# Kernel optimization log

Measured on AMD Instinct MI355X. Metric: run time of the kernel, lower is better.

## Reference

```python
import jax, jax.numpy as jnp
import numpy as np

B, T = 64, 4096
K = 67            # 25 body + 21 + 21 hand keypoints
D = 256           # first_layer_size
C = 7             # num_classes
THR = 0.1         # confidence_threshold
EPS = 1e-5        # BatchNorm eps


def setup_inputs() -> dict:
    key = jax.random.key(0)
    ks = jax.random.split(key, 8)
    body = jax.random.normal(ks[0], (B, T, 75), dtype=jnp.float32)
    hand_right = jax.random.normal(ks[1], (B, T, 63), dtype=jnp.float32)
    hand_left = jax.random.normal(ks[2], (B, T, 63), dtype=jnp.float32)
    length = jax.random.randint(ks[3], (B,), 1, T + 1, dtype=jnp.int64)
    W1 = jax.random.normal(ks[4], (2 * K, D), dtype=jnp.float32) * 0.05
    b1 = jnp.zeros((D,), dtype=jnp.float32)
    gamma = jnp.ones((D,), dtype=jnp.float32)
    beta = jnp.zeros((D,), dtype=jnp.float32)
    Wc = jax.random.normal(ks[5], (D, C), dtype=jnp.float32) * 0.05
    bc = jnp.zeros((C,), dtype=jnp.float32)
    return {"body": body, "hand_right": hand_right, "hand_left": hand_left,
            "length": length, "W1": W1, "b1": b1, "gamma": gamma,
            "beta": beta, "Wc": Wc, "bc": bc}


def reference(body, hand_right, hand_left, length, W1, b1, gamma, beta, Wc, bc):
    # concat keypoint streams -> [B, T, 3K] -> [B, T, K, 3]
    feats = jnp.concatenate([body, hand_right, hand_left], axis=2)
    feats = feats.reshape(feats.shape[0], feats.shape[1], -1, 3)
    x, y, conf = feats[..., 0], feats[..., 1], feats[..., 2]
    conf = (conf > THR).astype(feats.dtype)
    # gate coords by confidence, flatten to [B, T, 2K]
    pos = jnp.stack([x * conf, y * conf], axis=3)
    pos = pos.reshape(pos.shape[0], pos.shape[1], -1)
    # static MLP: Linear + ReLU -> [B, T, D]
    sf = jax.nn.relu(jnp.einsum("btf,fd->btd", pos, W1) + b1)
    # masked max pool over valid timesteps (vectorized segment-max)
    mask = jnp.arange(sf.shape[1])[None, :] < length[:, None]      # [B, T]
    pooled = jnp.max(jnp.where(mask[:, :, None], sf, -jnp.inf), axis=1)  # [B, D]
    # BatchNorm1d (training mode: batch statistics)
    mean = pooled.mean(axis=0)
    var = pooled.var(axis=0)
    bn = (pooled - mean) / jnp.sqrt(var + EPS) * gamma + beta
    # classifier
    return bn @ Wc + bc
```

## Files before the change

kernel.cpp:

```cpp
#include <hip/hip_runtime.h>
#include <hip/hip_bf16.h>

#define B_   64
#define T_   4096
#define K_   67
#define F_   134
#define FP_  160
#define D_   256
#define C_   7
#define THR_ 0.1f
#define EPS_ 1e-5f

typedef __bf16 bf16x8 __attribute__((ext_vector_type(8)));
typedef float  f32x4  __attribute__((ext_vector_type(4)));

typedef __attribute__((address_space(1))) const unsigned int guint;
typedef __attribute__((address_space(3))) unsigned int luint;


__device__ __forceinline__ int get_len(const int* L, int b) {
    return (L[1] == 0) ? L[2 * b] : L[b];
}

__global__ void convert_w1(const float* __restrict__ W1, __bf16* __restrict__ W1bf) {
    __shared__ float tile[32][33];
    const int d0 = blockIdx.x * 32, f0 = blockIdx.y * 32;
    const int tx = threadIdx.x & 31, ty = threadIdx.x >> 5;
#pragma unroll
    for (int r = 0; r < 32; r += 8) {
        int f = f0 + ty + r;
        tile[ty + r][tx] = (f < F_) ? W1[f * D_ + d0 + tx] : 0.f;
    }
    __syncthreads();
#pragma unroll
    for (int r = 0; r < 32; r += 8) {
        int d = d0 + ty + r;
        W1bf[d * FP_ + f0 + tx] = (__bf16)tile[tx][ty + r];
    }
}

__global__ __launch_bounds__(256, 3)
void fused_mlp_pool(const float* __restrict__ body,
                    const float* __restrict__ hr,
                    const float* __restrict__ hl,
                    const int*   __restrict__ length,
                    const float* __restrict__ b1,
                    const __bf16* __restrict__ W1bf,
                    float* __restrict__ pooled)
{
    const int b = blockIdx.y;
    const int len = get_len(length, b);
    const int t0 = blockIdx.x * 32;
    if (t0 >= len) return;

    __shared__ __align__(16) float  raw[6432];
    __shared__ __align__(16) __bf16 As[10 * 512];

    const int tid  = threadIdx.x;
    const int wave = tid >> 6;
    const int lane = tid & 63;
    const int quad = lane >> 4;
    const int l16  = lane & 15;
    const int dbase = wave * 64;

    const long rowb = (long)b * T_;
    const float* bodyt = body + (rowb + t0) * 75;
    const float* hrt   = hr   + (rowb + t0) * 63;
    const float* hlt   = hl   + (rowb + t0) * 63;

    for (int i = wave; i < 9; i += 4)
        __builtin_amdgcn_global_load_lds(
            (guint*)(bodyt + i * 256 + lane * 4),
            (luint*)((char*)raw + i * 1024 + lane * 16), 16, 0, 0);
    for (int i = wave; i < 7; i += 4)
        __builtin_amdgcn_global_load_lds(
            (guint*)(hrt + i * 256 + lane * 4),
            (luint*)((char*)raw + 9600 + i * 1024 + lane * 16), 16, 0, 0);
    for (int i = wave; i < 7; i += 4)
        __builtin_amdgcn_global_load_lds(
            (guint*)(hlt + i * 256 + lane * 4),
            (luint*)((char*)raw + 17664 + i * 1024 + lane * 16), 16, 0, 0);

    if (tid < 136) {
        const float* g; int loff;
        if (tid < 24)      { g = bodyt + 2304 + tid * 4;        loff = 2304 + tid * 4; }
        else if (tid < 80) { g = hrt + 1792 + (tid - 24) * 4;   loff = 4192 + (tid - 24) * 4; }
        else               { g = hlt + 1792 + (tid - 80) * 4;   loff = 6208 + (tid - 80) * 4; }
        *(float4*)(raw + loff) = *(const float4*)g;
    }

    bf16x8 bfrag[4][5];
    float  b1v[4];
#pragma unroll
    for (int n = 0; n < 4; n++) {
        int d = dbase + n * 16 + l16;
        const __bf16* p = W1bf + d * FP_ + quad * 8;
#pragma unroll
        for (int kt = 0; kt < 5; kt++)
            bfrag[n][kt] = *(const bf16x8*)(p + kt * 32);
        b1v[n] = b1[d];
    }

    for (int i = tid; i < 416; i += 256) {
        int t = i & 31, kp = 67 + (i >> 5);
        int w = ((t >> 4) * 5 + (kp >> 4)) * 256 + (((kp >> 2) & 3) * 16 + (t & 15)) * 4 + (kp & 3);
        ((unsigned int*)As)[w] = 0u;
    }
    __syncthreads();

#pragma unroll
    for (int it = 0; it < 8; it++) {
        int idx = it * 256 + tid;
        int t = (((idx >> 5) & 3) << 3) | ((idx >> 2) & 7);
        int k = (((idx >> 7) & 15) << 2) | (idx & 3);
        int roff;
        if (k < 25)      roff = t * 75 + 3 * k;
        else if (k < 46) roff = 2400 + t * 63 + 3 * (k - 25);
        else             roff = 4416 + t * 63 + 3 * (k - 46);
        float x = raw[roff], y = raw[roff + 1], cf = raw[roff + 2];
        if (!(cf > THR_)) { x = 0.f; y = 0.f; }
        unsigned short ux = __builtin_bit_cast(unsigned short, (__bf16)x);
        unsigned short uy = __builtin_bit_cast(unsigned short, (__bf16)y);
        int w = ((t >> 4) * 5 + (k >> 4)) * 256 + (((k >> 2) & 3) * 16 + (t & 15)) * 4 + (k & 3);
        ((unsigned int*)As)[w] = (unsigned int)ux | ((unsigned int)uy << 16);
    }
    if (tid < 96) {
        int t = tid & 31, k = 64 + (tid >> 5);
        int roff = 4416 + t * 63 + 3 * (k - 46);
        float x = raw[roff], y = raw[roff + 1], cf = raw[roff + 2];
        if (!(cf > THR_)) { x = 0.f; y = 0.f; }
        unsigned short ux = __builtin_bit_cast(unsigned short, (__bf16)x);
        unsigned short uy = __builtin_bit_cast(unsigned short, (__bf16)y);
        int w = ((t >> 4) * 5 + (k >> 4)) * 256 + (((k >> 2) & 3) * 16 + (t & 15)) * 4 + (k & 3);
        ((unsigned int*)As)[w] = (unsigned int)ux | ((unsigned int)uy << 16);
    }
    __syncthreads();

    f32x4 acc[2][4];
#pragma unroll
    for (int m = 0; m < 2; m++)
#pragma unroll
        for (int n = 0; n < 4; n++)
            acc[m][n] = (f32x4){0.f, 0.f, 0.f, 0.f};

#pragma unroll
    for (int kt = 0; kt < 5; kt++) {
#pragma unroll
        for (int m = 0; m < 2; m++) {
            bf16x8 a = *(const bf16x8*)(As + (m * 5 + kt) * 512 + lane * 8);
#pragma unroll
            for (int n = 0; n < 4; n++)
                acc[m][n] = __builtin_amdgcn_mfma_f32_16x16x32_bf16(a, bfrag[n][kt], acc[m][n], 0, 0, 0);
        }
    }

    float runmax[4] = {0.f, 0.f, 0.f, 0.f};
#pragma unroll
    for (int m = 0; m < 2; m++) {
        int trow0 = t0 + m * 16 + quad * 4;
#pragma unroll
        for (int r = 0; r < 4; r++) {
            bool valid = (trow0 + r) < len;
#pragma unroll
            for (int n = 0; n < 4; n++) {
                float v = acc[m][n][r] + b1v[n];
                v = (v > 0.f) ? v : 0.f;
                runmax[n] = (valid && v > runmax[n]) ? v : runmax[n];
            }
        }
    }
#pragma unroll
    for (int n = 0; n < 4; n++) {
        float r = runmax[n];
        r = fmaxf(r, __shfl_xor(r, 16, 64));
        r = fmaxf(r, __shfl_xor(r, 32, 64));
        if (quad == n) {
            atomicMax((unsigned int*)(pooled + b * D_ + dbase + n * 16 + l16),
                      __float_as_uint(r));
        }
    }
}

__global__ void bn_classifier(const float* __restrict__ pooled,
                              const float* __restrict__ gamma,
                              const float* __restrict__ beta,
                              const float* __restrict__ Wc,
                              const float* __restrict__ bc,
                              float* __restrict__ out)
{
    __shared__ float scale_s[D_], shift_s[D_];
    const int tid = threadIdx.x;
    float s = 0.f, ss = 0.f;
#pragma unroll 8
    for (int b = 0; b < B_; b++) {
        float v = pooled[b * D_ + tid];
        s += v; ss += v * v;
    }
    float mean = s * (1.f / B_);
    float var  = ss * (1.f / B_) - mean * mean;
    var = fmaxf(var, 0.f);
    float sc = gamma[tid] * rsqrtf(var + EPS_);
    scale_s[tid] = sc;
    shift_s[tid] = beta[tid] - mean * sc;

    const int wv = tid >> 6, ln = tid & 63;
    float wcr[4][C_];
#pragma unroll
    for (int j = 0; j < 4; j++)
#pragma unroll
        for (int c = 0; c < C_; c++)
            wcr[j][c] = Wc[(ln * 4 + j) * C_ + c];
    __syncthreads();

    for (int b = wv * 16; b < wv * 16 + 16; b++) {
        float4 v = *(const float4*)(pooled + b * D_ + ln * 4);
        float q[4];
        q[0] = v.x * scale_s[ln * 4 + 0] + shift_s[ln * 4 + 0];
        q[1] = v.y * scale_s[ln * 4 + 1] + shift_s[ln * 4 + 1];
        q[2] = v.z * scale_s[ln * 4 + 2] + shift_s[ln * 4 + 2];
        q[3] = v.w * scale_s[ln * 4 + 3] + shift_s[ln * 4 + 3];
        float p[C_];
#pragma unroll
        for (int c = 0; c < C_; c++) p[c] = 0.f;
#pragma unroll
        for (int j = 0; j < 4; j++)
#pragma unroll
            for (int c = 0; c < C_; c++)
                p[c] += q[j] * wcr[j][c];
#pragma unroll
        for (int c = 0; c < C_; c++) {
#pragma unroll
            for (int off = 1; off < 64; off <<= 1)
                p[c] += __shfl_xor(p[c], off, 64);
        }
        if (ln == 0) {
#pragma unroll
            for (int c = 0; c < C_; c++)
                out[b * C_ + c] = p[c] + bc[c];
        }
    }
}

extern "C" void kernel_launch(void* const* d_in, const int* in_sizes, int n_in,
                              void* d_out, int out_size, void* d_ws, size_t ws_size,
                              hipStream_t stream) {
    const float* body   = (const float*)d_in[0];
    const float* hr     = (const float*)d_in[1];
    const float* hl     = (const float*)d_in[2];
    const int*   length = (const int*)  d_in[3];
    const float* W1     = (const float*)d_in[4];
    const float* b1     = (const float*)d_in[5];
    const float* gamma  = (const float*)d_in[6];
    const float* beta   = (const float*)d_in[7];
    const float* Wc     = (const float*)d_in[8];
    const float* bc     = (const float*)d_in[9];
    float* out = (float*)d_out;

    float*  pooled = (float*)d_ws;
    __bf16* W1bf   = (__bf16*)((char*)d_ws + 65536);

    hipMemsetAsync(d_ws, 0, 65536, stream);
    convert_w1<<<dim3(8, 5), dim3(256), 0, stream>>>(W1, W1bf);
    fused_mlp_pool<<<dim3(128, B_), dim3(256), 0, stream>>>(body, hr, hl, length, b1, W1bf, pooled);
    bn_classifier<<<dim3(1), dim3(256), 0, stream>>>(pooled, gamma, beta, Wc, bc, out);
}
```

Measured before the change: 235.9 us.

## Use persistent grid over compacted valid tile list with amortized weight loads

Adds a small kernel that builds a compact list of valid (batch, time-tile) pairs from the lengths. The main kernel becomes a persistent grid of 1024 blocks that loops over this list. W1 fragments and bias are loaded once per block instead of once per tile, and blocks that would exit early are no longer launched. Occupancy hint raised to 4 blocks per CU. This adds an extra serial launch, and load/compute within a block are no longer overlapped across tiles.

Result: slower. 266.3 us (+12.9%).

```diff
diff --git a/kernel.cpp b/kernel.cpp
--- a/kernel.cpp
+++ b/kernel.cpp
@@ -10,6 +10,7 @@
 #define C_   7
 #define THR_ 0.1f
 #define EPS_ 1e-5f
+#define GRID_ 1024
 
 typedef __bf16 bf16x8 __attribute__((ext_vector_type(8)));
 typedef float  f32x4  __attribute__((ext_vector_type(4)));
@@ -39,22 +40,45 @@
     }
 }
 
-__global__ __launch_bounds__(256, 3)
+__global__ void build_tiles(const int* __restrict__ L,
+                            unsigned short* __restrict__ list,
+                            int* __restrict__ count) {
+    __shared__ int pref[65];
+    const int tid = threadIdx.x;
+    if (tid == 0) {
+        int acc = 0;
+        pref[0] = 0;
+        for (int b = 0; b < B_; b++) {
+            int len = (L[1] == 0) ? L[2 * b] : L[b];
+            acc += (len + 31) >> 5;
+            pref[b + 1] = acc;
+        }
+        *count = acc;
+    }
+    __syncthreads();
+    const int total = pref[64];
+    for (int i = tid; i < total; i += blockDim.x) {
+        int lo = 0, hi = 64;
+        while (hi - lo > 1) { int mid = (lo + hi) >> 1;
+                              if (pref[mid] <= i) lo = mid; else hi = mid; }
+        list[i] = (unsigned short)((lo << 7) | (i - pref[lo]));
+    }
+}
+
+__global__ __launch_bounds__(256, 4)
 void fused_mlp_pool(const float* __restrict__ body,
                     const float* __restrict__ hr,
                     const float* __restrict__ hl,
                     const int*   __restrict__ length,
                     const float* __restrict__ b1,
                     const __bf16* __restrict__ W1bf,
+                    const unsigned short* __restrict__ list,
+                    const int* __restrict__ count,
                     float* __restrict__ pooled)
 {
-    const int b = blockIdx.y;
-    const int len = get_len(length, b);
-    const int t0 = blockIdx.x * 32;
-    if (t0 >= len) return;
-
     __shared__ __align__(16) float  raw[6432];
     __shared__ __align__(16) __bf16 As[10 * 512];
+    __shared__ int len_s[B_];
 
     const int tid  = threadIdx.x;
     const int wave = tid >> 6;
@@ -63,31 +87,7 @@
     const int l16  = lane & 15;
     const int dbase = wave * 64;
 
-    const long rowb = (long)b * T_;
-    const float* bodyt = body + (rowb + t0) * 75;
-    const float* hrt   = hr   + (rowb + t0) * 63;
-    const float* hlt   = hl   + (rowb + t0) * 63;
-
-    for (int i = wave; i < 9; i += 4)
-        __builtin_amdgcn_global_load_lds(
-            (guint*)(bodyt + i * 256 + lane * 4),
-            (luint*)((char*)raw + i * 1024 + lane * 16), 16, 0, 0);
-    for (int i = wave; i < 7; i += 4)
-        __builtin_amdgcn_global_load_lds(
-            (guint*)(hrt + i * 256 + lane * 4),
-            (luint*)((char*)raw + 9600 + i * 1024 + lane * 16), 16, 0, 0);
-    for (int i = wave; i < 7; i += 4)
-        __builtin_amdgcn_global_load_lds(
-            (guint*)(hlt + i * 256 + lane * 4),
-            (luint*)((char*)raw + 17664 + i * 1024 + lane * 16), 16, 0, 0);
-
-    if (tid < 136) {
-        const float* g; int loff;
-        if (tid < 24)      { g = bodyt + 2304 + tid * 4;        loff = 2304 + tid * 4; }
-        else if (tid < 80) { g = hrt + 1792 + (tid - 24) * 4;   loff = 4192 + (tid - 24) * 4; }
-        else               { g = hlt + 1792 + (tid - 80) * 4;   loff = 6208 + (tid - 80) * 4; }
-        *(float4*)(raw + loff) = *(const float4*)g;
-    }
+    if (tid < B_) len_s[tid] = get_len(length, tid);
 
     bf16x8 bfrag[4][5];
     float  b1v[4];
@@ -106,77 +106,110 @@
         int w = ((t >> 4) * 5 + (kp >> 4)) * 256 + (((kp >> 2) & 3) * 16 + (t & 15)) * 4 + (kp & 3);
         ((unsigned int*)As)[w] = 0u;
     }
-    __syncthreads();
-
-#pragma unroll
-    for (int it = 0; it < 8; it++) {
-        int idx = it * 256 + tid;
-        int t = (((idx >> 5) & 3) << 3) | ((idx >> 2) & 7);
-        int k = (((idx >> 7) & 15) << 2) | (idx & 3);
-        int roff;
-        if (k < 25)      roff = t * 75 + 3 * k;
-        else if (k < 46) roff = 2400 + t * 63 + 3 * (k - 25);
-        else             roff = 4416 + t * 63 + 3 * (k - 46);
-        float x = raw[roff], y = raw[roff + 1], cf = raw[roff + 2];
-        if (!(cf > THR_)) { x = 0.f; y = 0.f; }
-        unsigned short ux = __builtin_bit_cast(unsigned short, (__bf16)x);
-        unsigned short uy = __builtin_bit_cast(unsigned short, (__bf16)y);
-        int w = ((t >> 4) * 5 + (k >> 4)) * 256 + (((k >> 2) & 3) * 16 + (t & 15)) * 4 + (k & 3);
-        ((unsigned int*)As)[w] = (unsigned int)ux | ((unsigned int)uy << 16);
-    }
-    if (tid < 96) {
-        int t = tid & 31, k = 64 + (tid >> 5);
-        int roff = 4416 + t * 63 + 3 * (k - 46);
-        float x = raw[roff], y = raw[roff + 1], cf = raw[roff + 2];
-        if (!(cf > THR_)) { x = 0.f; y = 0.f; }
-        unsigned short ux = __builtin_bit_cast(unsigned short, (__bf16)x);
-        unsigned short uy = __builtin_bit_cast(unsigned short, (__bf16)y);
-        int w = ((t >> 4) * 5 + (k >> 4)) * 256 + (((k >> 2) & 3) * 16 + (t & 15)) * 4 + (k & 3);
-        ((unsigned int*)As)[w] = (unsigned int)ux | ((unsigned int)uy << 16);
-    }
-    __syncthreads();
-
-    f32x4 acc[2][4];
-#pragma unroll
-    for (int m = 0; m < 2; m++)
-#pragma unroll
-        for (int n = 0; n < 4; n++)
-            acc[m][n] = (f32x4){0.f, 0.f, 0.f, 0.f};
-
-#pragma unroll
-    for (int kt = 0; kt < 5; kt++) {
+
+    const int total = *count;
+    for (int i = blockIdx.x; i < total; i += GRID_) {
+        const int e  = list[i];
+        const int b  = e >> 7;
+        const int t0 = (e & 127) << 5;
+        const long rowb = (long)b * T_;
+        const float* bodyt = body + (rowb + t0) * 75;
+        const float* hrt   = hr   + (rowb + t0) * 63;
+        const float* hlt   = hl   + (rowb + t0) * 63;
+
+        for (int k = wave; k < 9; k += 4)
+            __builtin_amdgcn_global_load_lds(
+                (guint*)(bodyt + k * 256 + lane * 4),
+                (luint*)((char*)raw + k * 1024 + lane * 16), 16, 0, 0);
+        for (int k = wave; k < 7; k += 4)
+            __builtin_amdgcn_global_load_lds(
+                (guint*)(hrt + k * 256 + lane * 4),
+                (luint*)((char*)raw + 9600 + k * 1024 + lane * 16), 16, 0, 0);
+        for (int k = wave; k < 7; k += 4)
+            __builtin_amdgcn_global_load_lds(
+                (guint*)(hlt + k * 256 + lane * 4),
+                (luint*)((char*)raw + 17664 + k * 1024 + lane * 16), 16, 0, 0);
+
+        if (tid < 136) {
+            const float* g; int loff;
+            if (tid < 24)      { g = bodyt + 2304 + tid * 4;        loff = 2304 + tid * 4; }
+            else if (tid < 80) { g = hrt + 1792 + (tid - 24) * 4;   loff = 4192 + (tid - 24) * 4; }
+            else               { g = hlt + 1792 + (tid - 80) * 4;   loff = 6208 + (tid - 80) * 4; }
+            *(float4*)(raw + loff) = *(const float4*)g;
+        }
+        __syncthreads();
+
+#pragma unroll
+        for (int it = 0; it < 8; it++) {
+            int idx = it * 256 + tid;
+            int t = (((idx >> 5) & 3) << 3) | ((idx >> 2) & 7);
+            int k = (((idx >> 7) & 15) << 2) | (idx & 3);
+            int roff;
+            if (k < 25)      roff = t * 75 + 3 * k;
+            else if (k < 46) roff = 2400 + t * 63 + 3 * (k - 25);
+            else             roff = 4416 + t * 63 + 3 * (k - 46);
+            float x = raw[roff], y = raw[roff + 1], cf = raw[roff + 2];
+            if (!(cf > THR_)) { x = 0.f; y = 0.f; }
+            unsigned short ux = __builtin_bit_cast(unsigned short, (__bf16)x);
+            unsigned short uy = __builtin_bit_cast(unsigned short, (__bf16)y);
+            int w = ((t >> 4) * 5 + (k >> 4)) * 256 + (((k >> 2) & 3) * 16 + (t & 15)) * 4 + (k & 3);
+            ((unsigned int*)As)[w] = (unsigned int)ux | ((unsigned int)uy << 16);
+        }
+        if (tid < 96) {
+            int t = tid & 31, k = 64 + (tid >> 5);
+            int roff = 4416 + t * 63 + 3 * (k - 46);
+            float x = raw[roff], y = raw[roff + 1], cf = raw[roff + 2];
+            if (!(cf > THR_)) { x = 0.f; y = 0.f; }
+            unsigned short ux = __builtin_bit_cast(unsigned short, (__bf16)x);
+            unsigned short uy = __builtin_bit_cast(unsigned short, (__bf16)y);
+            int w = ((t >> 4) * 5 + (k >> 4)) * 256 + (((k >> 2) & 3) * 16 + (t & 15)) * 4 + (k & 3);
+            ((unsigned int*)As)[w] = (unsigned int)ux | ((unsigned int)uy << 16);
+        }
+        __syncthreads();
+
+        f32x4 acc[2][4];
+#pragma unroll
+        for (int m = 0; m < 2; m++)
+#pragma unroll
+            for (int n = 0; n < 4; n++)
+                acc[m][n] = (f32x4){0.f, 0.f, 0.f, 0.f};
+
+#pragma unroll
+        for (int kt = 0; kt < 5; kt++) {
+#pragma unroll
+            for (int m = 0; m < 2; m++) {
+                bf16x8 a = *(const bf16x8*)(As + (m * 5 + kt) * 512 + lane * 8);
+#pragma unroll
+                for (int n = 0; n < 4; n++)
+                    acc[m][n] = __builtin_amdgcn_mfma_f32_16x16x32_bf16(a, bfrag[n][kt], acc[m][n], 0, 0, 0);
+            }
+        }
+
+        const int len = len_s[b];
+        float runmax[4] = {0.f, 0.f, 0.f, 0.f};
 #pragma unroll
         for (int m = 0; m < 2; m++) {
-            bf16x8 a = *(const bf16x8*)(As + (m * 5 + kt) * 512 + lane * 8);
-#pragma unroll
-            for (int n = 0; n < 4; n++)
-                acc[m][n] = __builtin_amdgcn_mfma_f32_16x16x32_bf16(a, bfrag[n][kt], acc[m][n], 0, 0, 0);
-        }
-    }
-
-    float runmax[4] = {0.f, 0.f, 0.f, 0.f};
-#pragma unroll
-    for (int m = 0; m < 2; m++) {
-        int trow0 = t0 + m * 16 + quad * 4;
-#pragma unroll
-        for (int r = 0; r < 4; r++) {
-            bool valid = (trow0 + r) < len;
-#pragma unroll
-            for (int n = 0; n < 4; n++) {
-                float v = acc[m][n][r] + b1v[n];
-                v = (v > 0.f) ? v : 0.f;
-                runmax[n] = (valid && v > runmax[n]) ? v : runmax[n];
+            int trow0 = t0 + m * 16 + quad * 4;
+#pragma unroll
+            for (int r = 0; r < 4; r++) {
+                bool valid = (trow0 + r) < len;
+#pragma unroll
+                for (int n = 0; n < 4; n++) {
+                    float v = acc[m][n][r] + b1v[n];
+                    v = (v > 0.f) ? v : 0.f;
+                    runmax[n] = (valid && v > runmax[n]) ? v : runmax[n];
+                }
             }
         }
-    }
-#pragma unroll
-    for (int n = 0; n < 4; n++) {
-        float r = runmax[n];
-        r = fmaxf(r, __shfl_xor(r, 16, 64));
-        r = fmaxf(r, __shfl_xor(r, 32, 64));
-        if (quad == n) {
-            atomicMax((unsigned int*)(pooled + b * D_ + dbase + n * 16 + l16),
-                      __float_as_uint(r));
+#pragma unroll
+        for (int n = 0; n < 4; n++) {
+            float r = runmax[n];
+            r = fmaxf(r, __shfl_xor(r, 16, 64));
+            r = fmaxf(r, __shfl_xor(r, 32, 64));
+            if (quad == n) {
+                atomicMax((unsigned int*)(pooled + b * D_ + dbase + n * 16 + l16),
+                          __float_as_uint(r));
+            }
         }
     }
 }
@@ -256,11 +289,15 @@
     const float* bc     = (const float*)d_in[9];
     float* out = (float*)d_out;
 
-    float*  pooled = (float*)d_ws;
-    __bf16* W1bf   = (__bf16*)((char*)d_ws + 65536);
+    float*          pooled = (float*)d_ws;
+    __bf16*         W1bf   = (__bf16*)((char*)d_ws + 65536);
+    unsigned short* list   = (unsigned short*)((char*)d_ws + 147456);
+    int*            count  = (int*)((char*)d_ws + 163840);
 
     hipMemsetAsync(d_ws, 0, 65536, stream);
     convert_w1<<<dim3(8, 5), dim3(256), 0, stream>>>(W1, W1bf);
-    fused_mlp_pool<<<dim3(128, B_), dim3(256), 0, stream>>>(body, hr, hl, length, b1, W1bf, pooled);
+    build_tiles<<<dim3(1), dim3(256), 0, stream>>>(length, list, count);
+    fused_mlp_pool<<<dim3(GRID_), dim3(256), 0, stream>>>(body, hr, hl, length, b1,
+                                                          W1bf, list, count, pooled);
     bn_classifier<<<dim3(1), dim3(256), 0, stream>>>(pooled, gamma, beta, Wc, bc, out);
 }
```

## Process four time tiles per block with double-buffered async LDS prefetch

Applied to the files above, without the earlier changes.

Each block now walks up to four 32-timestep chunks instead of one. While the current chunk is converted to bf16 and run through MFMA, the next chunk's keypoint data is prefetched into a second LDS buffer. This amortizes the W1 fragment loads, the bias loads and the per-block atomicMax over more work, and overlaps global loads with compute. In exchange LDS use doubles and occupancy is lowered to two blocks per CU. With four times fewer blocks there is also less parallelism and coarser load balance across batches of varying length.

Result: slower. 246.0 us (+4.2%).

```diff
diff --git a/kernel.cpp b/kernel.cpp
--- a/kernel.cpp
+++ b/kernel.cpp
@@ -10,6 +10,7 @@
 #define C_   7
 #define THR_ 0.1f
 #define EPS_ 1e-5f
+#define TPB_ 4
 
 typedef __bf16 bf16x8 __attribute__((ext_vector_type(8)));
 typedef float  f32x4  __attribute__((ext_vector_type(4)));
@@ -39,7 +40,7 @@
     }
 }
 
-__global__ __launch_bounds__(256, 3)
+__global__ __launch_bounds__(256, 2)
 void fused_mlp_pool(const float* __restrict__ body,
                     const float* __restrict__ hr,
                     const float* __restrict__ hl,
@@ -50,10 +51,11 @@
 {
     const int b = blockIdx.y;
     const int len = get_len(length, b);
-    const int t0 = blockIdx.x * 32;
-    if (t0 >= len) return;
-
-    __shared__ __align__(16) float  raw[6432];
+    const int cbase = blockIdx.x * (TPB_ * 32);
+    if (cbase >= len) return;
+    const int nt = min(TPB_, (len - cbase + 31) >> 5);
+
+    __shared__ __align__(16) float  raw[2][6432];
     __shared__ __align__(16) __bf16 As[10 * 512];
 
     const int tid  = threadIdx.x;
@@ -64,30 +66,34 @@
     const int dbase = wave * 64;
 
     const long rowb = (long)b * T_;
-    const float* bodyt = body + (rowb + t0) * 75;
-    const float* hrt   = hr   + (rowb + t0) * 63;
-    const float* hlt   = hl   + (rowb + t0) * 63;
-
-    for (int i = wave; i < 9; i += 4)
-        __builtin_amdgcn_global_load_lds(
-            (guint*)(bodyt + i * 256 + lane * 4),
-            (luint*)((char*)raw + i * 1024 + lane * 16), 16, 0, 0);
-    for (int i = wave; i < 7; i += 4)
-        __builtin_amdgcn_global_load_lds(
-            (guint*)(hrt + i * 256 + lane * 4),
-            (luint*)((char*)raw + 9600 + i * 1024 + lane * 16), 16, 0, 0);
-    for (int i = wave; i < 7; i += 4)
-        __builtin_amdgcn_global_load_lds(
-            (guint*)(hlt + i * 256 + lane * 4),
-            (luint*)((char*)raw + 17664 + i * 1024 + lane * 16), 16, 0, 0);
-
-    if (tid < 136) {
-        const float* g; int loff;
-        if (tid < 24)      { g = bodyt + 2304 + tid * 4;        loff = 2304 + tid * 4; }
-        else if (tid < 80) { g = hrt + 1792 + (tid - 24) * 4;   loff = 4192 + (tid - 24) * 4; }
-        else               { g = hlt + 1792 + (tid - 80) * 4;   loff = 6208 + (tid - 80) * 4; }
-        *(float4*)(raw + loff) = *(const float4*)g;
-    }
+
+    auto issue = [&](int tt, float* rbuf) {
+        const float* bt = body + (rowb + cbase + tt * 32) * 75;
+        const float* ht = hr   + (rowb + cbase + tt * 32) * 63;
+        const float* lt = hl   + (rowb + cbase + tt * 32) * 63;
+        for (int k = wave; k < 9; k += 4)
+            __builtin_amdgcn_global_load_lds(
+                (guint*)(bt + k * 256 + lane * 4),
+                (luint*)((char*)rbuf + k * 1024 + lane * 16), 16, 0, 0);
+        for (int k = wave; k < 7; k += 4)
+            __builtin_amdgcn_global_load_lds(
+                (guint*)(ht + k * 256 + lane * 4),
+                (luint*)((char*)rbuf + 9600 + k * 1024 + lane * 16), 16, 0, 0);
+        for (int k = wave; k < 7; k += 4)
+            __builtin_amdgcn_global_load_lds(
+                (guint*)(lt + k * 256 + lane * 4),
+                (luint*)((char*)rbuf + 17664 + k * 1024 + lane * 16), 16, 0, 0);
+    };
+    auto tail_ptr = [&](int tt, int& loff) -> const float* {
+        const long base = (rowb + cbase + tt * 32);
+        if (tid < 24)  { loff = 2304 + tid * 4;        return body + base * 75 + 2304 + tid * 4; }
+        if (tid < 80)  { loff = 4192 + (tid - 24) * 4; return hr + base * 63 + 1792 + (tid - 24) * 4; }
+        loff = 6208 + (tid - 80) * 4;                  return hl + base * 63 + 1792 + (tid - 80) * 4;
+    };
+
+    issue(0, raw[0]);
+    if (tid < 136) { int lo; const float4 v = *(const float4*)tail_ptr(0, lo);
+                     *(float4*)(raw[0] + lo) = v; }
 
     bf16x8 bfrag[4][5];
     float  b1v[4];
@@ -108,67 +114,86 @@
     }
     __syncthreads();
 
-#pragma unroll
-    for (int it = 0; it < 8; it++) {
-        int idx = it * 256 + tid;
-        int t = (((idx >> 5) & 3) << 3) | ((idx >> 2) & 7);
-        int k = (((idx >> 7) & 15) << 2) | (idx & 3);
-        int roff;
-        if (k < 25)      roff = t * 75 + 3 * k;
-        else if (k < 46) roff = 2400 + t * 63 + 3 * (k - 25);
-        else             roff = 4416 + t * 63 + 3 * (k - 46);
-        float x = raw[roff], y = raw[roff + 1], cf = raw[roff + 2];
-        if (!(cf > THR_)) { x = 0.f; y = 0.f; }
-        unsigned short ux = __builtin_bit_cast(unsigned short, (__bf16)x);
-        unsigned short uy = __builtin_bit_cast(unsigned short, (__bf16)y);
-        int w = ((t >> 4) * 5 + (k >> 4)) * 256 + (((k >> 2) & 3) * 16 + (t & 15)) * 4 + (k & 3);
-        ((unsigned int*)As)[w] = (unsigned int)ux | ((unsigned int)uy << 16);
-    }
-    if (tid < 96) {
-        int t = tid & 31, k = 64 + (tid >> 5);
-        int roff = 4416 + t * 63 + 3 * (k - 46);
-        float x = raw[roff], y = raw[roff + 1], cf = raw[roff + 2];
-        if (!(cf > THR_)) { x = 0.f; y = 0.f; }
-        unsigned short ux = __builtin_bit_cast(unsigned short, (__bf16)x);
-        unsigned short uy = __builtin_bit_cast(unsigned short, (__bf16)y);
-        int w = ((t >> 4) * 5 + (k >> 4)) * 256 + (((k >> 2) & 3) * 16 + (t & 15)) * 4 + (k & 3);
-        ((unsigned int*)As)[w] = (unsigned int)ux | ((unsigned int)uy << 16);
-    }
-    __syncthreads();
-
-    f32x4 acc[2][4];
-#pragma unroll
-    for (int m = 0; m < 2; m++)
-#pragma unroll
-        for (int n = 0; n < 4; n++)
-            acc[m][n] = (f32x4){0.f, 0.f, 0.f, 0.f};
-
-#pragma unroll
-    for (int kt = 0; kt < 5; kt++) {
+    float runmax[4] = {0.f, 0.f, 0.f, 0.f};
+    int cur = 0;
+
+    for (int c = 0; c < nt; c++) {
+        float4 tailv;
+        int    tailoff = 0;
+        const bool pre = (c + 1 < nt);
+        if (pre) {
+            issue(c + 1, raw[cur ^ 1]);
+            if (tid < 136) tailv = *(const float4*)tail_ptr(c + 1, tailoff);
+        }
+
+        const float* rb = raw[cur];
+#pragma unroll
+        for (int it = 0; it < 8; it++) {
+            int idx = it * 256 + tid;
+            int t = (((idx >> 5) & 3) << 3) | ((idx >> 2) & 7);
+            int k = (((idx >> 7) & 15) << 2) | (idx & 3);
+            int roff;
+            if (k < 25)      roff = t * 75 + 3 * k;
+            else if (k < 46) roff = 2400 + t * 63 + 3 * (k - 25);
+            else             roff = 4416 + t * 63 + 3 * (k - 46);
+            float x = rb[roff], y = rb[roff + 1], cf = rb[roff + 2];
+            if (!(cf > THR_)) { x = 0.f; y = 0.f; }
+            unsigned short ux = __builtin_bit_cast(unsigned short, (__bf16)x);
+            unsigned short uy = __builtin_bit_cast(unsigned short, (__bf16)y);
+            int w = ((t >> 4) * 5 + (k >> 4)) * 256 + (((k >> 2) & 3) * 16 + (t & 15)) * 4 + (k & 3);
+            ((unsigned int*)As)[w] = (unsigned int)ux | ((unsigned int)uy << 16);
+        }
+        if (tid < 96) {
+            int t = tid & 31, k = 64 + (tid >> 5);
+            int roff = 4416 + t * 63 + 3 * (k - 46);
+            float x = rb[roff], y = rb[roff + 1], cf = rb[roff + 2];
+            if (!(cf > THR_)) { x = 0.f; y = 0.f; }
+            unsigned short ux = __builtin_bit_cast(unsigned short, (__bf16)x);
+            unsigned short uy = __builtin_bit_cast(unsigned short, (__bf16)y);
+            int w = ((t >> 4) * 5 + (k >> 4)) * 256 + (((k >> 2) & 3) * 16 + (t & 15)) * 4 + (k & 3);
+            ((unsigned int*)As)[w] = (unsigned int)ux | ((unsigned int)uy << 16);
+        }
+        __syncthreads();
+
+        if (pre && tid < 136) *(float4*)(raw[cur ^ 1] + tailoff) = tailv;
+
+        f32x4 acc[2][4];
+#pragma unroll
+        for (int m = 0; m < 2; m++)
+#pragma unroll
+            for (int n = 0; n < 4; n++)
+                acc[m][n] = (f32x4){0.f, 0.f, 0.f, 0.f};
+#pragma unroll
+        for (int kt = 0; kt < 5; kt++) {
+            bf16x8 a0 = *(const bf16x8*)(As + (0 * 5 + kt) * 512 + lane * 8);
+            bf16x8 a1 = *(const bf16x8*)(As + (1 * 5 + kt) * 512 + lane * 8);
+#pragma unroll
+            for (int n = 0; n < 4; n++) {
+                acc[0][n] = __builtin_amdgcn_mfma_f32_16x16x32_bf16(a0, bfrag[n][kt], acc[0][n], 0, 0, 0);
+                acc[1][n] = __builtin_amdgcn_mfma_f32_16x16x32_bf16(a1, bfrag[n][kt], acc[1][n], 0, 0, 0);
+            }
+        }
+
+        const int t0 = cbase + c * 32;
 #pragma unroll
         for (int m = 0; m < 2; m++) {
-            bf16x8 a = *(const bf16x8*)(As + (m * 5 + kt) * 512 + lane * 8);
-#pragma unroll
-            for (int n = 0; n < 4; n++)
-                acc[m][n] = __builtin_amdgcn_mfma_f32_16x16x32_bf16(a, bfrag[n][kt], acc[m][n], 0, 0, 0);
-        }
-    }
-
-    float runmax[4] = {0.f, 0.f, 0.f, 0.f};
-#pragma unroll
-    for (int m = 0; m < 2; m++) {
-        int trow0 = t0 + m * 16 + quad * 4;
-#pragma unroll
-        for (int r = 0; r < 4; r++) {
-            bool valid = (trow0 + r) < len;
-#pragma unroll
-            for (int n = 0; n < 4; n++) {
-                float v = acc[m][n][r] + b1v[n];
-                v = (v > 0.f) ? v : 0.f;
-                runmax[n] = (valid && v > runmax[n]) ? v : runmax[n];
+            int trow0 = t0 + m * 16 + quad * 4;
+#pragma unroll
+            for (int r = 0; r < 4; r++) {
+                bool valid = (trow0 + r) < len;
+#pragma unroll
+                for (int n = 0; n < 4; n++) {
+                    float v = acc[m][n][r] + b1v[n];
+                    v = (v > 0.f) ? v : 0.f;
+                    runmax[n] = (valid && v > runmax[n]) ? v : runmax[n];
+                }
             }
         }
-    }
+
+        if (c + 1 < nt) __syncthreads();
+        cur ^= 1;
+    }
+
 #pragma unroll
     for (int n = 0; n < 4; n++) {
         float r = runmax[n];
@@ -261,6 +286,7 @@
 
     hipMemsetAsync(d_ws, 0, 65536, stream);
     convert_w1<<<dim3(8, 5), dim3(256), 0, stream>>>(W1, W1bf);
-    fused_mlp_pool<<<dim3(128, B_), dim3(256), 0, stream>>>(body, hr, hl, length, b1, W1bf, pooled);
+    fused_mlp_pool<<<dim3(32, B_), dim3(256), 0, stream>>>(body, hr, hl, length, b1,
+                                                           W1bf, pooled);
     bn_classifier<<<dim3(1), dim3(256), 0, stream>>>(pooled, gamma, beta, Wc, bc, out);
 }
```
